# Optimization experiments

Measured on AMD Instinct MI355X. Metric: run time of the kernel, lower is better.

## Reference

```python
import jax, jax.numpy as jnp
import numpy as np

N, IN_F, OUT_F = 2048, 512, 512

def setup_inputs() -> dict:
    key = jax.random.key(0)
    kx, ka, kb = jax.random.split(key, 3)
    x = jax.random.uniform(kx, (N, IN_F), dtype=jnp.float32)          # inputs in [0,1]
    a = jax.random.uniform(ka, (OUT_F, IN_F), dtype=jnp.float32)      # weight in [0,1]
    b = jax.random.uniform(kb, (OUT_F,), dtype=jnp.float32)           # bias in [0,1]
    return {"x": x, "a": a, "b": b}

def reference(x, a, b):
    # Lukasiewicz / max-plus 'matmul':
    # y[n,o] = max(0, max_i(x[n,i] + a[o,i] - 1)), then max with bias b[o].
    inter = x[:, None, :] + a[None, :, :] - 1.0        # [N, out, in]
    y = jnp.maximum(jnp.max(inter, axis=-1), 0.0)      # [N, out]
    y = jnp.maximum(y, b[None, :])
    return y
```

## Files before the change

kernel.cpp:

```cpp
#include <hip/hip_runtime.h>
#include <cstdint>


#define NROW 2048
#define NK   512
#define NCOL 512
#define RPB  16
#define CB   64
#define NW   8
#define KQ   16
typedef float f32x4 __attribute__((ext_vector_type(4)));

__device__ __forceinline__ void async_load16(const float* g, float* l) {
  __builtin_amdgcn_global_load_lds(
      (const __attribute__((address_space(1))) void*)g,
      (__attribute__((address_space(3))) void*)l, 16, 0, 0);
}

__global__ __launch_bounds__(256) void luka_prep(const float* __restrict__ A,
                                                 f32x4* __restrict__ Apb) {
  int idx = blockIdx.x * 256 + threadIdx.x;
  int o  = idx >> 7;
  int k4 = idx & 127;
  f32x4 v = *(const f32x4*)(A + o * NK + k4 * 4);
  Apb[(((o >> 6) * 128) + k4) * 64 + (o & 63)] = v;
}

__global__ __launch_bounds__(512, 8) void luka_main(
    const f32x4* __restrict__ Apb, const float* __restrict__ X,
    const float* __restrict__ Bv, float* __restrict__ Y) {
  __shared__ float lds[RPB * NK];
  const int tid  = threadIdx.x;
  const int lane = tid & 63;
  const int w    = tid >> 6;
  const int colblk  = blockIdx.x;
  const int rowBase = blockIdx.y * RPB;

  {
    const float* Xg = X + (size_t)rowBase * NK;
#pragma unroll
    for (int rnd = 0; rnd < 4; ++rnd) {
      int base = rnd * 512 + w * 64;
      async_load16(Xg + (size_t)(base + lane) * 4, &lds[base * 4]);
    }
  }

  const f32x4* __restrict__ Aw =
      Apb + ((size_t)(colblk * 128 + w * KQ) * 64 + lane);

  float acc[RPB];
#pragma unroll
  for (int r = 0; r < RPB; ++r) acc[r] = 0.0f;

  __syncthreads();

#pragma unroll 2
  for (int j = 0; j < KQ; ++j) {
    const f32x4 av = Aw[j * 64];
    const int kb = (w * KQ + j) * 4;
#pragma unroll
    for (int r = 0; r < RPB; ++r) {
      const f32x4 xv = *(const f32x4*)&lds[r * NK + kb];
      f32x4 s = av + xv;
      acc[r] = fmaxf(fmaxf(s.x, s.y), acc[r]);
      acc[r] = fmaxf(fmaxf(s.z, s.w), acc[r]);
    }
  }

  __syncthreads();
#pragma unroll
  for (int r = 0; r < RPB; ++r) lds[(w * RPB + r) * CB + lane] = acc[r];
  __syncthreads();

  const float bv = Bv[colblk * CB + lane];
#pragma unroll
  for (int i = 0; i < 2; ++i) {
    const int r = w * 2 + i;
    float m0 = fmaxf(fmaxf(lds[(0 * RPB + r) * CB + lane],
                           lds[(1 * RPB + r) * CB + lane]),
                     fmaxf(lds[(2 * RPB + r) * CB + lane],
                           lds[(3 * RPB + r) * CB + lane]));
    float m1 = fmaxf(fmaxf(lds[(4 * RPB + r) * CB + lane],
                           lds[(5 * RPB + r) * CB + lane]),
                     fmaxf(lds[(6 * RPB + r) * CB + lane],
                           lds[(7 * RPB + r) * CB + lane]));
    float t = fmaxf(m0, m1) - 1.0f;
    Y[(size_t)(rowBase + r) * NCOL + colblk * CB + lane] =
        fmaxf(fmaxf(t, bv), 0.0f);
  }
}

#define TILE 64
#define BK   64
__global__ __launch_bounds__(256) void luka_fb(
    const float* __restrict__ X, const float* __restrict__ A,
    const float* __restrict__ Bv, float* __restrict__ Y) {
  __shared__ float xs[2][TILE * BK];
  __shared__ float as[2][TILE * BK];
  const int tid = threadIdx.x, wave = tid >> 6, tx = tid & 15, ty = tid >> 4;
  const int rowBase = blockIdx.y * TILE, colBase = blockIdx.x * TILE;
  uint32_t xoff[4], aoff[4];
#pragma unroll
  for (int r = 0; r < 4; ++r) {
    int row = ty * 4 + r;
    xoff[r] = (uint32_t)row * 256u + ((uint32_t)((row & 15) ^ (row >> 2)) << 4);
  }
#pragma unroll
  for (int c = 0; c < 4; ++c) {
    int row = tx * 4 + c;
    aoff[c] = (uint32_t)row * 256u + ((uint32_t)((row & 15) ^ (row >> 2)) << 4);
  }
  float acc[4][4];
#pragma unroll
  for (int r = 0; r < 4; ++r)
#pragma unroll
    for (int c = 0; c < 4; ++c) acc[r][c] = 0.0f;
  const int row0 = tid >> 4, sl = tid & 15;
  auto stage = [&](int buf, int kt) {
#pragma unroll
    for (int j = 0; j < 4; ++j) {
      int row = row0 + j * 16;
      int m = (row & 15) ^ (row >> 2);
      int kk = ((sl ^ m) << 2);
      async_load16(X + (size_t)(rowBase + row) * NK + kt * BK + kk,
                   &xs[buf][j * 1024 + wave * 256]);
      async_load16(A + (size_t)(colBase + row) * NK + kt * BK + kk,
                   &as[buf][j * 1024 + wave * 256]);
    }
  };
  stage(0, 0);
  __syncthreads();
  int buf = 0;
#pragma unroll 1
  for (int kt = 0; kt < NK / BK; ++kt) {
    if (kt < NK / BK - 1) stage(buf ^ 1, kt + 1);
    const char* xb = (const char*)&xs[buf][0];
    const char* ab = (const char*)&as[buf][0];
#pragma unroll
    for (int s4 = 0; s4 < BK / 4; ++s4) {
      f32x4 xf[4], af[4];
#pragma unroll
      for (int r = 0; r < 4; ++r)
        xf[r] = *(const f32x4*)(xb + (xoff[r] ^ (uint32_t)(s4 << 4)));
#pragma unroll
      for (int c = 0; c < 4; ++c)
        af[c] = *(const f32x4*)(ab + (aoff[c] ^ (uint32_t)(s4 << 4)));
#pragma unroll
      for (int r = 0; r < 4; ++r)
#pragma unroll
        for (int c = 0; c < 4; ++c) {
          f32x4 s = xf[r] + af[c];
          float t0 = fmaxf(fmaxf(s.x, s.y), acc[r][c]);
          acc[r][c] = fmaxf(fmaxf(s.z, s.w), t0);
        }
    }
    __syncthreads();
    buf ^= 1;
  }
  const f32x4 bv = *(const f32x4*)&Bv[colBase + tx * 4];
  float bvv[4] = {bv.x, bv.y, bv.z, bv.w};
#pragma unroll
  for (int r = 0; r < 4; ++r) {
    f32x4 o;
    o.x = fmaxf(fmaxf(acc[r][0] - 1.0f, bvv[0]), 0.0f);
    o.y = fmaxf(fmaxf(acc[r][1] - 1.0f, bvv[1]), 0.0f);
    o.z = fmaxf(fmaxf(acc[r][2] - 1.0f, bvv[2]), 0.0f);
    o.w = fmaxf(fmaxf(acc[r][3] - 1.0f, bvv[3]), 0.0f);
    *(f32x4*)&Y[(size_t)(rowBase + ty * 4 + r) * NCOL + colBase + tx * 4] = o;
  }
}

extern "C" void kernel_launch(void* const* d_in, const int* in_sizes, int n_in,
                              void* d_out, int out_size, void* d_ws, size_t ws_size,
                              hipStream_t stream) {
  const float* X = (const float*)d_in[0];
  const float* A = (const float*)d_in[1];
  const float* B = (const float*)d_in[2];
  float* Y = (float*)d_out;

  if (ws_size >= (size_t)NCOL * NK * sizeof(float)) {
    f32x4* Apb = (f32x4*)d_ws;
    luka_prep<<<dim3(NCOL * NK / 4 / 256), dim3(256), 0, stream>>>(A, Apb);
    dim3 grid(NCOL / CB, NROW / RPB);
    luka_main<<<grid, dim3(512), 0, stream>>>(Apb, X, B, Y);
  } else {
    dim3 grid(NCOL / TILE, NROW / TILE);
    luka_fb<<<grid, dim3(256), 0, stream>>>(X, A, B, Y);
  }
}
```

Before: 87.96 us.

## Widen column block to 128 so each thread reuses X loads across two columns

Each thread now accumulates two output columns, so every LDS read of X feeds two A vectors. The column block doubles to 128, which halves the grid's column dimension, and the prep layout changes to match. The reduction epilogue is restructured into two halves that stage partial maxima through LDS. This is meant to cut LDS traffic per max-plus op, at the cost of twice the accumulator registers and lower declared occupancy (min blocks per CU goes from 8 to 4).

```diff
diff --git a/kernel.cpp b/kernel.cpp
--- a/kernel.cpp
+++ b/kernel.cpp
@@ -6,8 +6,7 @@
 #define NK   512
 #define NCOL 512
 #define RPB  16
-#define CB   64
-#define NW   8
+#define CBL  128
 #define KQ   16
 typedef float f32x4 __attribute__((ext_vector_type(4)));
 
@@ -23,10 +22,10 @@
   int o  = idx >> 7;
   int k4 = idx & 127;
   f32x4 v = *(const f32x4*)(A + o * NK + k4 * 4);
-  Apb[(((o >> 6) * 128) + k4) * 64 + (o & 63)] = v;
+  Apb[(((o >> 7) * 128) + k4) * 128 + (o & 127)] = v;
 }
 
-__global__ __launch_bounds__(512, 8) void luka_main(
+__global__ __launch_bounds__(512, 4) void luka_main(
     const f32x4* __restrict__ Apb, const float* __restrict__ X,
     const float* __restrict__ Bv, float* __restrict__ Y) {
   __shared__ float lds[RPB * NK];
@@ -46,47 +45,54 @@
   }
 
   const f32x4* __restrict__ Aw =
-      Apb + ((size_t)(colblk * 128 + w * KQ) * 64 + lane);
+      Apb + ((size_t)(colblk * 128 + w * KQ) * 128 + lane);
 
-  float acc[RPB];
+  float acc[RPB][2];
 #pragma unroll
-  for (int r = 0; r < RPB; ++r) acc[r] = 0.0f;
+  for (int r = 0; r < RPB; ++r) { acc[r][0] = 0.0f; acc[r][1] = 0.0f; }
 
   __syncthreads();
 
-#pragma unroll 2
+#pragma unroll 4
   for (int j = 0; j < KQ; ++j) {
-    const f32x4 av = Aw[j * 64];
+    const f32x4 a0 = Aw[j * 128];
+    const f32x4 a1 = Aw[j * 128 + 64];
     const int kb = (w * KQ + j) * 4;
 #pragma unroll
     for (int r = 0; r < RPB; ++r) {
       const f32x4 xv = *(const f32x4*)&lds[r * NK + kb];
-      f32x4 s = av + xv;
-      acc[r] = fmaxf(fmaxf(s.x, s.y), acc[r]);
-      acc[r] = fmaxf(fmaxf(s.z, s.w), acc[r]);
+      f32x4 s0 = a0 + xv;
+      f32x4 s1 = a1 + xv;
+      acc[r][0] = fmaxf(fmaxf(s0.x, s0.y), acc[r][0]);
+      acc[r][0] = fmaxf(fmaxf(s0.z, s0.w), acc[r][0]);
+      acc[r][1] = fmaxf(fmaxf(s1.x, s1.y), acc[r][1]);
+      acc[r][1] = fmaxf(fmaxf(s1.z, s1.w), acc[r][1]);
     }
   }
 
+  const float bv = Bv[colblk * CBL + (tid & 127)];
   __syncthreads();
+#pragma unroll 1
+  for (int half = 0; half < 2; ++half) {
 #pragma unroll
-  for (int r = 0; r < RPB; ++r) lds[(w * RPB + r) * CB + lane] = acc[r];
-  __syncthreads();
-
-  const float bv = Bv[colblk * CB + lane];
+    for (int r = 0; r < 8; ++r) {
+      lds[(w * 8 + r) * CBL + lane]      = acc[half * 8 + r][0];
+      lds[(w * 8 + r) * CBL + 64 + lane] = acc[half * 8 + r][1];
+    }
+    __syncthreads();
 #pragma unroll
-  for (int i = 0; i < 2; ++i) {
-    const int r = w * 2 + i;
-    float m0 = fmaxf(fmaxf(lds[(0 * RPB + r) * CB + lane],
-                           lds[(1 * RPB + r) * CB + lane]),
-                     fmaxf(lds[(2 * RPB + r) * CB + lane],
-                           lds[(3 * RPB + r) * CB + lane]));
-    float m1 = fmaxf(fmaxf(lds[(4 * RPB + r) * CB + lane],
-                           lds[(5 * RPB + r) * CB + lane]),
-                     fmaxf(lds[(6 * RPB + r) * CB + lane],
-                           lds[(7 * RPB + r) * CB + lane]));
-    float t = fmaxf(m0, m1) - 1.0f;
-    Y[(size_t)(rowBase + r) * NCOL + colblk * CB + lane] =
-        fmaxf(fmaxf(t, bv), 0.0f);
+    for (int e0 = 0; e0 < 2; ++e0) {
+      int e   = e0 * 512 + tid;
+      int row = e >> 7, col = e & 127;
+      float m = lds[row * CBL + col];
+#pragma unroll
+      for (int ww = 1; ww < 8; ++ww)
+        m = fmaxf(m, lds[(ww * 8 + row) * CBL + col]);
+      float t = m - 1.0f;
+      Y[(size_t)(rowBase + half * 8 + row) * NCOL + colblk * CBL + col] =
+          fmaxf(fmaxf(t, bv), 0.0f);
+    }
+    __syncthreads();
   }
 }
 
@@ -181,7 +187,7 @@
   if (ws_size >= (size_t)NCOL * NK * sizeof(float)) {
     f32x4* Apb = (f32x4*)d_ws;
     luka_prep<<<dim3(NCOL * NK / 4 / 256), dim3(256), 0, stream>>>(A, Apb);
-    dim3 grid(NCOL / CB, NROW / RPB);
+    dim3 grid(NCOL / CBL, NROW / RPB);
     luka_main<<<grid, dim3(512), 0, stream>>>(Apb, X, B, Y);
   } else {
     dim3 grid(NCOL / TILE, NROW / TILE);
```

Result: faster. 84.45 us (-4.0%).
